# Kernel tuning notes

Hardware: AMD Instinct MI355X
Metric: run time of the kernel (lower is better)

## Reference

```python
import jax, jax.numpy as jnp
import numpy as np

N = 50000
E = 1600000
NEG_SLOPE = 0.2
BN_EPS = 1e-5


def gat_conv(x, src, dst, W, a_s, a_d, b):
    """PyG-style GATConv (concat=True). a_s/a_d: [H, C]."""
    H, C = a_s.shape
    h = (x @ W).reshape(-1, H, C)  # [N, H, C]
    alpha_src = jnp.einsum('nhc,hc->nh', h, a_s)  # [N, H]
    alpha_dst = jnp.einsum('nhc,hc->nh', h, a_d)  # [N, H]
    e = jax.nn.leaky_relu(alpha_src[src] + alpha_dst[dst], NEG_SLOPE)  # [E, H]
    # segment softmax over edges sharing the same destination node
    m = jax.ops.segment_max(e, dst, num_segments=N)
    e = jnp.exp(e - m[dst])
    s = jax.ops.segment_sum(e, dst, num_segments=N)
    alpha = e / (s[dst] + 1e-16)  # [E, H]
    msg = h[src] * alpha[:, :, None]  # [E, H, C]
    out = jax.ops.segment_sum(msg, dst, num_segments=N)  # [N, H, C]
    return out.reshape(-1, H * C) + b


def batch_norm(x, g, beta):
    mu = jnp.mean(x, axis=0)
    var = jnp.var(x, axis=0)
    return (x - mu) * jax.lax.rsqrt(var + BN_EPS) * g + beta


def setup_inputs() -> dict:
    key = jax.random.key(0)
    ks = jax.random.split(key, 20)
    d_in, hid, heads, d_out = 128, 16, 4, 40
    hh = hid * heads  # 64
    inp = {
        'x': jax.random.normal(ks[0], (N, d_in), jnp.float32),
        'edge_index': jax.random.randint(ks[1], (2, E), 0, N, jnp.int32),
        # layer 0: in -> hid*heads
        'W0': jax.random.normal(ks[2], (d_in, hh), jnp.float32) * 0.05,
        'a_src0': jax.random.normal(ks[3], (heads, hid), jnp.float32) * 0.05,
        'a_dst0': jax.random.normal(ks[4], (heads, hid), jnp.float32) * 0.05,
        'b0': jnp.zeros((hh,), jnp.float32),
        'g0': jnp.ones((hh,), jnp.float32),
        'beta0': jnp.zeros((hh,), jnp.float32),
        # layer 1: hid*heads -> hid*heads
        'W1': jax.random.normal(ks[5], (hh, hh), jnp.float32) * 0.1,
        'a_src1': jax.random.normal(ks[6], (heads, hid), jnp.float32) * 0.1,
        'a_dst1': jax.random.normal(ks[7], (heads, hid), jnp.float32) * 0.1,
        'b1': jnp.zeros((hh,), jnp.float32),
        'g1': jnp.ones((hh,), jnp.float32),
        'beta1': jnp.zeros((hh,), jnp.float32),
        # layer 2: hid*heads -> out, heads=1
        'W2': jax.random.normal(ks[8], (hh, d_out), jnp.float32) * 0.1,
        'a_src2': jax.random.normal(ks[9], (1, d_out), jnp.float32) * 0.1,
        'a_dst2': jax.random.normal(ks[10], (1, d_out), jnp.float32) * 0.1,
        'b2': jnp.zeros((d_out,), jnp.float32),
    }
    return inp


def reference(x, edge_index, W0, a_src0, a_dst0, b0, g0, beta0,
              W1, a_src1, a_dst1, b1, g1, beta1,
              W2, a_src2, a_dst2, b2):
    # add self-loops (PyG GATConv default)
    loop = jnp.arange(N, dtype=edge_index.dtype)
    src = jnp.concatenate([edge_index[0], loop])
    dst = jnp.concatenate([edge_index[1], loop])

    h = gat_conv(x, src, dst, W0, a_src0, a_dst0, b0)
    h = jax.nn.relu(batch_norm(h, g0, beta0))
    h = gat_conv(h, src, dst, W1, a_src1, a_dst1, b1)
    h = jax.nn.relu(batch_norm(h, g1, beta1))
    h = gat_conv(h, src, dst, W2, a_src2, a_dst2, b2)
    return jax.nn.log_softmax(h, axis=-1)
```

## Files before the change

kernel.cpp:

```cpp
#include <hip/hip_runtime.h>
#include <math.h>

#define NEG_SLOPE 0.2f
#define CAP 128
#define BCAP 6144

__device__ __forceinline__ unsigned enc_f(float f) {
    unsigned b = __float_as_uint(f);
    return (b & 0x80000000u) ? ~b : (b | 0x80000000u);
}
__device__ __forceinline__ float dec_f(unsigned u) {
    return (u & 0x80000000u) ? __uint_as_float(u ^ 0x80000000u) : __uint_as_float(~u);
}
#define ENC_NEG_INF 0x007FFFFFu

__device__ __forceinline__ unsigned short f2bf(float f) {
    unsigned u = __float_as_uint(f);
    u += 0x7fffu + ((u >> 16) & 1u);
    return (unsigned short)(u >> 16);
}
__device__ __forceinline__ float bf2f(unsigned short b) {
    return __uint_as_float(((unsigned)b) << 16);
}

static inline int nblk(long total, int b) { return (int)((total + b - 1) / b); }

__global__ void init_kernel(int* bincnt, float* bn, unsigned* menc, int nbin) {
    int i = blockIdx.x * blockDim.x + threadIdx.x;
    if (i < nbin) bincnt[i] = 0;
    if (i < 256) bn[i] = 0.f;
    if (i < 16) menc[i] = ENC_NEG_INF;
}

__global__ void bin_kernel(const int* __restrict__ srcs, const int* __restrict__ dsts,
                           int E_, int EA, int nbin, int* bincnt, unsigned* __restrict__ binbuf) {
    __shared__ int lh[512];
    __shared__ int lbase[512];
    int tid = threadIdx.x;
    for (int i = tid; i < nbin; i += 256) lh[i] = 0;
    __syncthreads();
    int chunk = (EA + gridDim.x - 1) / gridDim.x;
    int e0 = blockIdx.x * chunk;
    int e1 = e0 + chunk; if (e1 > EA) e1 = EA;
    for (int i = e0 + tid; i < e1; i += 256) {
        int d = (i < E_) ? dsts[i] : (i - E_);
        atomicAdd(&lh[d >> 7], 1);
    }
    __syncthreads();
    for (int i = tid; i < nbin; i += 256) {
        lbase[i] = atomicAdd(&bincnt[i], lh[i]);
        lh[i] = 0;
    }
    __syncthreads();
    for (int i = e0 + tid; i < e1; i += 256) {
        int s, d;
        if (i < E_) { s = srcs[i]; d = dsts[i]; } else { s = d = i - E_; }
        int b = d >> 7;
        int pos = lbase[b] + atomicAdd(&lh[b], 1);
        if (pos < BCAP) binbuf[(size_t)b * BCAP + pos] = ((unsigned)s << 16) | (unsigned)d;
    }
}

__global__ void build_kernel(const unsigned* __restrict__ binbuf, const int* __restrict__ bincnt,
                             unsigned short* __restrict__ esrc, int* __restrict__ cnt, int n) {
    __shared__ unsigned short slab[128 * CAP];
    __shared__ int lcnt[128];
    int tid = threadIdx.x;
    int b = blockIdx.x, d0 = b << 7;
    if (tid < 128) lcnt[tid] = 0;
    __syncthreads();
    int nb = bincnt[b]; if (nb > BCAP) nb = BCAP;
    for (int i = tid; i < nb; i += 256) {
        unsigned u = binbuf[(size_t)b * BCAP + i];
        int s = (int)(u >> 16);
        int ld = (int)(u & 0xffffu) - d0;
        int pos = atomicAdd(&lcnt[ld], 1);
        if (pos < CAP) slab[ld * CAP + pos] = (unsigned short)s;
    }
    __syncthreads();
    const uint4* sl = (const uint4*)slab;
    uint4* outp = (uint4*)esrc;
    for (int i = tid; i < 128 * CAP / 8; i += 256) {
        int r = i >> 4;
        if (d0 + r < n) outp[(size_t)(d0 + r) * (CAP / 8) + (i & 15)] = sl[i];
    }
    if (tid < 128 && d0 + tid < n) cnt[d0 + tid] = lcnt[tid];
}

template <int K, bool BN>
__global__ __launch_bounds__(256) void gemm_alpha_kernel(
    const float* __restrict__ X, const float* __restrict__ W,
    const float* __restrict__ a_s, const float* __restrict__ a_d,
    unsigned short* __restrict__ Hout, float* __restrict__ as_o,
    float* __restrict__ ad_o, unsigned* menc_, int n,
    const float* __restrict__ bnsum, const float* __restrict__ bnsq,
    const float* __restrict__ g, const float* __restrict__ beta) {
    __shared__ float Xs[32][132];
    __shared__ float Ws[32][64];
    __shared__ float scale[BN ? K : 4];
    __shared__ float shift[BN ? K : 4];
    __shared__ float redm[4][4];

    int tid = threadIdx.x;
    if (BN) {
        if (tid < K) {
            float inv_n = 1.0f / (float)n;
            float mu = bnsum[tid] * inv_n;
            float var = bnsq[tid] * inv_n - mu * mu;
            float sc = rsqrtf(var + 1e-5f) * g[tid];
            scale[tid] = sc;
            shift[tid] = beta[tid] - mu * sc;
        }
        __syncthreads();
    }

    int node0 = blockIdx.x * 128;
    int tx = tid & 7;
    int ty = tid >> 3;

    int snode = tid & 127;
    int khalf = (tid >> 7) * 16;
    int src_row = node0 + snode; if (src_row >= n) src_row = n - 1;
    const float* xrow = X + (size_t)src_row * K;

    float acc[4][8];
#pragma unroll
    for (int i = 0; i < 4; ++i)
#pragma unroll
        for (int j = 0; j < 8; ++j) acc[i][j] = 0.f;

    constexpr int NCH = K / 32;
    for (int c = 0; c < NCH; ++c) {
        int k0 = c * 32;
#pragma unroll
        for (int r = 0; r < 2; ++r) {
            int f = tid + r * 256;
            int kk = f >> 4;
            int cq = f & 15;
            float4 wv4 = *(const float4*)(W + (size_t)(k0 + kk) * 64 + cq * 4);
            *(float4*)&Ws[kk][cq * 4] = wv4;
        }
#pragma unroll
        for (int q = 0; q < 4; ++q) {
            int kk = khalf + q * 4;
            float4 v = *(const float4*)(xrow + k0 + kk);
            if (BN) {
                float4 sc = *(const float4*)(&scale[k0 + kk]);
                float4 sh = *(const float4*)(&shift[k0 + kk]);
                v.x = fmaxf(fmaf(v.x, sc.x, sh.x), 0.f);
                v.y = fmaxf(fmaf(v.y, sc.y, sh.y), 0.f);
                v.z = fmaxf(fmaf(v.z, sc.z, sh.z), 0.f);
                v.w = fmaxf(fmaf(v.w, sc.w, sh.w), 0.f);
            }
            Xs[kk + 0][snode] = v.x;
            Xs[kk + 1][snode] = v.y;
            Xs[kk + 2][snode] = v.z;
            Xs[kk + 3][snode] = v.w;
        }
        __syncthreads();
#pragma unroll 2
        for (int kk = 0; kk < 32; ++kk) {
            float4 xv = *(const float4*)(&Xs[kk][ty * 4]);
            float4 wa = *(const float4*)(&Ws[kk][tx * 8]);
            float4 wb = *(const float4*)(&Ws[kk][tx * 8 + 4]);
            float xs_[4] = {xv.x, xv.y, xv.z, xv.w};
            float ws_[8] = {wa.x, wa.y, wa.z, wa.w, wb.x, wb.y, wb.z, wb.w};
#pragma unroll
            for (int i = 0; i < 4; ++i)
#pragma unroll
                for (int j = 0; j < 8; ++j)
                    acc[i][j] = fmaf(xs_[i], ws_[j], acc[i][j]);
        }
        __syncthreads();
    }

    float4 asa = *(const float4*)(a_s + tx * 8);
    float4 asb = *(const float4*)(a_s + tx * 8 + 4);
    float4 ada = *(const float4*)(a_d + tx * 8);
    float4 adb = *(const float4*)(a_d + tx * 8 + 4);
    int head = tx >> 1;
    float p1v[4], p2v[4];
#pragma unroll
    for (int i = 0; i < 4; ++i) {
        float p1 = acc[i][0] * asa.x + acc[i][1] * asa.y + acc[i][2] * asa.z + acc[i][3] * asa.w
                 + acc[i][4] * asb.x + acc[i][5] * asb.y + acc[i][6] * asb.z + acc[i][7] * asb.w;
        float p2 = acc[i][0] * ada.x + acc[i][1] * ada.y + acc[i][2] * ada.z + acc[i][3] * ada.w
                 + acc[i][4] * adb.x + acc[i][5] * adb.y + acc[i][6] * adb.z + acc[i][7] * adb.w;
        p1 += __shfl_xor(p1, 1, 64);
        p2 += __shfl_xor(p2, 1, 64);
        p1v[i] = p1; p2v[i] = p2;
    }
#pragma unroll
    for (int i = 0; i < 4; ++i) {
        int node = node0 + ty * 4 + i;
        if (node < n) {
            unsigned r0 = (unsigned)f2bf(acc[i][0]) | ((unsigned)f2bf(acc[i][1]) << 16);
            unsigned r1 = (unsigned)f2bf(acc[i][2]) | ((unsigned)f2bf(acc[i][3]) << 16);
            unsigned r2 = (unsigned)f2bf(acc[i][4]) | ((unsigned)f2bf(acc[i][5]) << 16);
            unsigned r3 = (unsigned)f2bf(acc[i][6]) | ((unsigned)f2bf(acc[i][7]) << 16);
            *(uint4*)(Hout + (size_t)node * 64 + tx * 8) = make_uint4(r0, r1, r2, r3);
            if ((tx & 1) == 0) {
                as_o[(size_t)node * 4 + head] = p1v[i];
                ad_o[(size_t)node * 4 + head] = p2v[i];
            }
        }
    }
    float am = -1e30f;
    if ((tx & 1) == 0)
        am = fmaxf(fmaxf(p1v[0], p1v[1]), fmaxf(p1v[2], p1v[3]));
    am = fmaxf(am, __shfl_xor(am, 8, 64));
    am = fmaxf(am, __shfl_xor(am, 16, 64));
    am = fmaxf(am, __shfl_xor(am, 32, 64));
    int lane = tid & 63;
    if (lane < 8 && (lane & 1) == 0) redm[tid >> 6][lane >> 1] = am;
    __syncthreads();
    if (tid < 4) {
        float m = fmaxf(fmaxf(redm[0][tid], redm[1][tid]), fmaxf(redm[2][tid], redm[3][tid]));
        atomicMax(&menc_[tid], enc_f(m));
    }
}

__global__ void gather64_kernel(const int* __restrict__ cnt,
                                const unsigned short* __restrict__ esrc,
                                const float* __restrict__ as_, const float* __restrict__ ad_,
                                const unsigned short* __restrict__ Hf,
                                const unsigned* __restrict__ menc,
                                const float* __restrict__ bias, float* __restrict__ feat, int n) {
    int tid = threadIdx.x;
    int wv = tid >> 6, lane = tid & 63;
    int slot = lane >> 4, ql = lane & 15;
    int r8 = lane >> 3, qc = lane & 7;
    int node = blockIdx.x * 4 + wv;
    if (node >= n) return;

    int deg = cnt[node]; if (deg > CAP) deg = CAP;
    const unsigned short* ep = esrc + (size_t)node * CAP;
    float4 adv4 = *(const float4*)(ad_ + (size_t)node * 4);
    float adh = (slot == 0) ? adv4.x : (slot == 1) ? adv4.y : (slot == 2) ? adv4.z : adv4.w;
    float mm = dec_f(menc[slot]) + adh;
    float mh = mm > 0.f ? mm : NEG_SLOPE * mm;

    float4 accA = make_float4(0.f, 0.f, 0.f, 0.f);
    float4 accB = make_float4(0.f, 0.f, 0.f, 0.f);
    float wp = 0.f;
    int nch = (deg + 15) >> 4;

    int lim0 = deg < 16 ? deg : 16;
    int s0 = (ql < lim0) ? (int)ep[ql] : 0;
    float aA = as_[(unsigned)(s0 * 4 + slot)];
    int sA = 0;
    if (nch > 1) {
        int l1 = deg - 16; if (l1 > 16) l1 = 16;
        sA = (ql < l1) ? (int)ep[16 + ql] : 0;
    }
    uint4 hA0, hA1, hB0, hB1;
    {
        int sj0 = __shfl(s0, r8, 64);
        hA0 = *(const uint4*)(Hf + (unsigned)(sj0 * 64 + qc * 8));
        int sj1 = __shfl(s0, 8 + r8, 64);
        hA1 = *(const uint4*)(Hf + (unsigned)(sj1 * 64 + qc * 8));
    }
    hB0 = hA0; hB1 = hA1;
    int sB = 0; float aB = 0.f;

#define G64_FMA8(H0, WJ)                                                  \
    accA.x = fmaf(bf2f((unsigned short)(H0.x)), WJ, accA.x);              \
    accA.y = fmaf(bf2f((unsigned short)(H0.x >> 16)), WJ, accA.y);        \
    accA.z = fmaf(bf2f((unsigned short)(H0.y)), WJ, accA.z);              \
    accA.w = fmaf(bf2f((unsigned short)(H0.y >> 16)), WJ, accA.w);        \
    accB.x = fmaf(bf2f((unsigned short)(H0.z)), WJ, accB.x);              \
    accB.y = fmaf(bf2f((unsigned short)(H0.z >> 16)), WJ, accB.y);        \
    accB.z = fmaf(bf2f((unsigned short)(H0.w)), WJ, accB.z);              \
    accB.w = fmaf(bf2f((unsigned short)(H0.w >> 16)), WJ, accB.w);

#define G64_CHUNK(c, hC0, hC1, hN0, hN1, sC, sN, aC, aN)                      \
    {                                                                         \
        int lim = deg - (c) * 16; if (lim > 16) lim = 16;                     \
        float ev = aC + adh;                                                  \
        ev = ev > 0.f ? ev : NEG_SLOPE * ev;                                  \
        float w = (ql < lim) ? __expf(ev - mh) : 0.f;                         \
        if ((c) + 1 < nch) aN = as_[(unsigned)(sC * 4 + slot)];               \
        if ((c) + 2 < nch) {                                                  \
            int l2 = deg - ((c) + 2) * 16; if (l2 > 16) l2 = 16;              \
            sN = (ql < l2) ? (int)ep[((c) + 2) * 16 + ql] : 0;                \
        }                                                                     \
        if ((c) + 1 < nch) {                                                  \
            int sj0 = __shfl(sC, r8, 64);                                     \
            hN0 = *(const uint4*)(Hf + (unsigned)(sj0 * 64 + qc * 8));        \
            int sj1 = __shfl(sC, 8 + r8, 64);                                 \
            hN1 = *(const uint4*)(Hf + (unsigned)(sj1 * 64 + qc * 8));        \
        }                                                                     \
        wp += w;                                                              \
        {                                                                     \
            float wj = __shfl(w, ((qc >> 1) << 4) + r8, 64);                  \
            G64_FMA8(hC0, wj)                                                 \
        }                                                                     \
        if (lim > 8) {                                                        \
            float wj = __shfl(w, ((qc >> 1) << 4) + 8 + r8, 64);              \
            G64_FMA8(hC1, wj)                                                 \
        }                                                                     \
    }

    for (int c = 0; c < nch; c += 2) {
        G64_CHUNK(c, hA0, hA1, hB0, hB1, sA, sB, aA, aB);
        if (c + 1 < nch) G64_CHUNK(c + 1, hB0, hB1, hA0, hA1, sB, sA, aB, aA);
    }
#undef G64_CHUNK
#undef G64_FMA8

#pragma unroll
    for (int o = 8; o < 64; o <<= 1) {
        accA.x += __shfl_xor(accA.x, o, 64);
        accA.y += __shfl_xor(accA.y, o, 64);
        accA.z += __shfl_xor(accA.z, o, 64);
        accA.w += __shfl_xor(accA.w, o, 64);
        accB.x += __shfl_xor(accB.x, o, 64);
        accB.y += __shfl_xor(accB.y, o, 64);
        accB.z += __shfl_xor(accB.z, o, 64);
        accB.w += __shfl_xor(accB.w, o, 64);
    }
#pragma unroll
    for (int o = 1; o < 16; o <<= 1) wp += __shfl_xor(wp, o, 64);
    float wsh = __shfl(wp, ((lane & 7) >> 1) << 4, 64);
    if (lane < 8) {
        float inv = 1.0f / (wsh + 1e-16f);
        float4 bv0 = *(const float4*)(bias + lane * 8);
        float4 bv1 = *(const float4*)(bias + lane * 8 + 4);
        float4 r0, r1;
        r0.x = fmaf(accA.x, inv, bv0.x);
        r0.y = fmaf(accA.y, inv, bv0.y);
        r0.z = fmaf(accA.z, inv, bv0.z);
        r0.w = fmaf(accA.w, inv, bv0.w);
        r1.x = fmaf(accB.x, inv, bv1.x);
        r1.y = fmaf(accB.y, inv, bv1.y);
        r1.z = fmaf(accB.z, inv, bv1.z);
        r1.w = fmaf(accB.w, inv, bv1.w);
        *(float4*)(feat + (size_t)node * 64 + lane * 8) = r0;
        *(float4*)(feat + (size_t)node * 64 + lane * 8 + 4) = r1;
    }
}

__global__ void prep2_kernel(const float* __restrict__ feat, const float* __restrict__ bnsum,
                             const float* __restrict__ bnsq, const float* __restrict__ g,
                             const float* __restrict__ beta, const float* __restrict__ W2,
                             const float* __restrict__ as2v, const float* __restrict__ ad2v,
                             unsigned short* __restrict__ z, float* __restrict__ as_o,
                             float* __restrict__ ad_o, unsigned* menc_, int n) {
    __shared__ float sc[64], sh[64], vs[64], vd[64];
    int tid = threadIdx.x;
    if (tid < 64) {
        float inv_n = 1.0f / (float)n;
        float mu = bnsum[tid] * inv_n;
        float var = bnsq[tid] * inv_n - mu * mu;
        float s = rsqrtf(var + 1e-5f) * g[tid];
        sc[tid] = s;
        sh[tid] = beta[tid] - mu * s;
    } else if (tid < 128) {
        int k = tid - 64;
        float s1 = 0.f, s2 = 0.f;
        for (int j = 0; j < 40; ++j) {
            float wv = W2[k * 40 + j];
            s1 = fmaf(wv, as2v[j], s1);
            s2 = fmaf(wv, ad2v[j], s2);
        }
        vs[k] = s1;
        vd[k] = s2;
    }
    __syncthreads();
    int lane = tid & 63, wv = tid >> 6;
    float scl = sc[lane], shl = sh[lane], vsl = vs[lane], vdl = vd[lane];
    float amax = -1e30f;
    int nwaves = gridDim.x * 4;
    for (int node = blockIdx.x * 4 + wv; node < n; node += nwaves) {
        float v = fmaf(feat[(size_t)node * 64 + lane], scl, shl);
        v = v > 0.f ? v : 0.f;
        z[(size_t)node * 64 + lane] = f2bf(v);
        float p1 = v * vsl, p2 = v * vdl;
#pragma unroll
        for (int o = 1; o < 64; o <<= 1) {
            p1 += __shfl_xor(p1, o, 64);
            p2 += __shfl_xor(p2, o, 64);
        }
        amax = fmaxf(amax, p1);
        if (lane == 0) { as_o[node] = p1; ad_o[node] = p2; }
    }
    if (lane == 0) atomicMax(menc_, enc_f(amax));
}

__global__ void gatherz_kernel(const int* __restrict__ cnt,
                               const unsigned short* __restrict__ esrc,
                               const float* __restrict__ as_, const float* __restrict__ ad_,
                               const unsigned short* __restrict__ Z,
                               const unsigned* __restrict__ menc,
                               float* __restrict__ agg, int n) {
    int tid = threadIdx.x;
    int wv = tid >> 6, lane = tid & 63;
    int r8 = lane >> 3, qc = lane & 7;
    int node = blockIdx.x * 4 + wv;
    if (node >= n) return;

    int deg = cnt[node]; if (deg > CAP) deg = CAP;
    const unsigned short* ep = esrc + (size_t)node * CAP;
    float adv = ad_[node];
    float mm = dec_f(menc[0]) + adv;
    float mh = mm > 0.f ? mm : NEG_SLOPE * mm;

    float4 accA = make_float4(0.f, 0.f, 0.f, 0.f);
    float4 accB = make_float4(0.f, 0.f, 0.f, 0.f);
    float wp = 0.f;
    for (int base = 0; base < deg; base += 64) {
        int lim = deg - base; if (lim > 64) lim = 64;
        int s = 0;
        if (lane < lim) s = (int)ep[base + lane];
        float asv = (lane < lim) ? as_[(unsigned)s] : 0.f;
        uint4 hv[8];
#pragma unroll
        for (int i = 0; i < 8; ++i) {
            if (i * 8 >= lim) break;
            int sj = __shfl(s, i * 8 + r8, 64);
            hv[i] = *(const uint4*)(Z + (unsigned)(sj * 64 + qc * 8));
        }
        float w = 0.f;
        if (lane < lim) {
            float ev = asv + adv;
            ev = ev > 0.f ? ev : NEG_SLOPE * ev;
            w = __expf(ev - mh);
        }
        wp += w;
#pragma unroll
        for (int i = 0; i < 8; ++i) {
            if (i * 8 >= lim) break;
            float wj = __shfl(w, i * 8 + r8, 64);
            uint4 h4 = hv[i];
            accA.x = fmaf(bf2f((unsigned short)(h4.x)), wj, accA.x);
            accA.y = fmaf(bf2f((unsigned short)(h4.x >> 16)), wj, accA.y);
            accA.z = fmaf(bf2f((unsigned short)(h4.y)), wj, accA.z);
            accA.w = fmaf(bf2f((unsigned short)(h4.y >> 16)), wj, accA.w);
            accB.x = fmaf(bf2f((unsigned short)(h4.z)), wj, accB.x);
            accB.y = fmaf(bf2f((unsigned short)(h4.z >> 16)), wj, accB.y);
            accB.z = fmaf(bf2f((unsigned short)(h4.w)), wj, accB.z);
            accB.w = fmaf(bf2f((unsigned short)(h4.w >> 16)), wj, accB.w);
        }
    }
#pragma unroll
    for (int o = 8; o < 64; o <<= 1) {
        accA.x += __shfl_xor(accA.x, o, 64);
        accA.y += __shfl_xor(accA.y, o, 64);
        accA.z += __shfl_xor(accA.z, o, 64);
        accA.w += __shfl_xor(accA.w, o, 64);
        accB.x += __shfl_xor(accB.x, o, 64);
        accB.y += __shfl_xor(accB.y, o, 64);
        accB.z += __shfl_xor(accB.z, o, 64);
        accB.w += __shfl_xor(accB.w, o, 64);
    }
#pragma unroll
    for (int o = 1; o < 64; o <<= 1) wp += __shfl_xor(wp, o, 64);
    if (lane < 8) {
        float inv = 1.0f / (wp + 1e-16f);
        float4 r0, r1;
        r0.x = accA.x * inv; r0.y = accA.y * inv; r0.z = accA.z * inv; r0.w = accA.w * inv;
        r1.x = accB.x * inv; r1.y = accB.y * inv; r1.z = accB.z * inv; r1.w = accB.w * inv;
        *(float4*)(agg + (size_t)node * 64 + lane * 8) = r0;
        *(float4*)(agg + (size_t)node * 64 + lane * 8 + 4) = r1;
    }
}

__global__ __launch_bounds__(256) void gemm_lsm_kernel(const float* __restrict__ X,
                                                       const float* __restrict__ W,
                                                       const float* __restrict__ bias,
                                                       float* __restrict__ out, int n) {
    __shared__ float Xs[32][132];
    __shared__ float Ws[32][40];
    __shared__ float bs[40];
    int tid = threadIdx.x;
    if (tid < 40) bs[tid] = bias[tid];

    int node0 = blockIdx.x * 128;
    int tx = tid & 7;
    int ty = tid >> 3;
    int snode = tid & 127;
    int khalf = (tid >> 7) * 16;
    int src_row = node0 + snode; if (src_row >= n) src_row = n - 1;
    const float* xrow = X + (size_t)src_row * 64;

    float acc[4][5];
#pragma unroll
    for (int i = 0; i < 4; ++i)
#pragma unroll
        for (int j = 0; j < 5; ++j) acc[i][j] = 0.f;

    for (int c = 0; c < 2; ++c) {
        int k0 = c * 32;
        for (int f = tid; f < 320; f += 256) {
            int kk = f / 10, q = f - kk * 10;
            *(float4*)&Ws[kk][q * 4] = *(const float4*)(W + (size_t)(k0 + kk) * 40 + q * 4);
        }
#pragma unroll
        for (int q = 0; q < 4; ++q) {
            int kk = khalf + q * 4;
            float4 v = *(const float4*)(xrow + k0 + kk);
            Xs[kk + 0][snode] = v.x;
            Xs[kk + 1][snode] = v.y;
            Xs[kk + 2][snode] = v.z;
            Xs[kk + 3][snode] = v.w;
        }
        __syncthreads();
#pragma unroll 2
        for (int kk = 0; kk < 32; ++kk) {
            float4 xv = *(const float4*)(&Xs[kk][ty * 4]);
            float w0 = Ws[kk][tx * 5 + 0];
            float w1 = Ws[kk][tx * 5 + 1];
            float w2 = Ws[kk][tx * 5 + 2];
            float w3 = Ws[kk][tx * 5 + 3];
            float w4 = Ws[kk][tx * 5 + 4];
            float xs_[4] = {xv.x, xv.y, xv.z, xv.w};
#pragma unroll
            for (int i = 0; i < 4; ++i) {
                acc[i][0] = fmaf(xs_[i], w0, acc[i][0]);
                acc[i][1] = fmaf(xs_[i], w1, acc[i][1]);
                acc[i][2] = fmaf(xs_[i], w2, acc[i][2]);
                acc[i][3] = fmaf(xs_[i], w3, acc[i][3]);
                acc[i][4] = fmaf(xs_[i], w4, acc[i][4]);
            }
        }
        __syncthreads();
    }

    float b0 = bs[tx * 5 + 0], b1 = bs[tx * 5 + 1], b2 = bs[tx * 5 + 2],
          b3 = bs[tx * 5 + 3], b4 = bs[tx * 5 + 4];
#pragma unroll
    for (int i = 0; i < 4; ++i) {
        float v0 = acc[i][0] + b0, v1 = acc[i][1] + b1, v2 = acc[i][2] + b2,
              v3 = acc[i][3] + b3, v4 = acc[i][4] + b4;
        float m = fmaxf(fmaxf(fmaxf(v0, v1), fmaxf(v2, v3)), v4);
        m = fmaxf(m, __shfl_xor(m, 1, 64));
        m = fmaxf(m, __shfl_xor(m, 2, 64));
        m = fmaxf(m, __shfl_xor(m, 4, 64));
        float ex = __expf(v0 - m) + __expf(v1 - m) + __expf(v2 - m)
                 + __expf(v3 - m) + __expf(v4 - m);
        ex += __shfl_xor(ex, 1, 64);
        ex += __shfl_xor(ex, 2, 64);
        ex += __shfl_xor(ex, 4, 64);
        float ls = m + logf(ex);
        int node = node0 + ty * 4 + i;
        if (node < n) {
            float* op = out + (size_t)node * 40 + tx * 5;
            op[0] = v0 - ls;
            op[1] = v1 - ls;
            op[2] = v2 - ls;
            op[3] = v3 - ls;
            op[4] = v4 - ls;
        }
    }
}

__global__ void bn_stats_kernel(const float* __restrict__ feat, float* bnsum, float* bnsq,
                                int n) {
    __shared__ float ls[256], lq[256];
    int f = threadIdx.x & 63, y = threadIdx.x >> 6;
    float ps = 0.f, pq = 0.f;
    for (int node = blockIdx.x * 4 + y; node < n; node += gridDim.x * 4) {
        float v = feat[(size_t)node * 64 + f];
        ps += v;
        pq += v * v;
    }
    ls[threadIdx.x] = ps;
    lq[threadIdx.x] = pq;
    __syncthreads();
    if (y == 0) {
        atomicAdd(&bnsum[f], ls[f] + ls[f + 64] + ls[f + 128] + ls[f + 192]);
        atomicAdd(&bnsq[f], lq[f] + lq[f + 64] + lq[f + 128] + lq[f + 192]);
    }
}

extern "C" void kernel_launch(void* const* d_in, const int* in_sizes, int n_in,
                              void* d_out, int out_size, void* d_ws, size_t ws_size,
                              hipStream_t stream) {
    const float* x   = (const float*)d_in[0];
    const int*   ei  = (const int*)d_in[1];
    const float* W0  = (const float*)d_in[2];
    const float* as0 = (const float*)d_in[3];
    const float* ad0 = (const float*)d_in[4];
    const float* b0  = (const float*)d_in[5];
    const float* g0  = (const float*)d_in[6];
    const float* be0 = (const float*)d_in[7];
    const float* W1  = (const float*)d_in[8];
    const float* as1 = (const float*)d_in[9];
    const float* ad1 = (const float*)d_in[10];
    const float* b1  = (const float*)d_in[11];
    const float* g1  = (const float*)d_in[12];
    const float* be1 = (const float*)d_in[13];
    const float* W2  = (const float*)d_in[14];
    const float* as2 = (const float*)d_in[15];
    const float* ad2 = (const float*)d_in[16];
    const float* b2  = (const float*)d_in[17];

    const int N  = in_sizes[0] / 128;
    const int E  = in_sizes[1] / 2;
    const int EA = E + N;
    const int NBIN = (N + 127) >> 7;
    const int* srcs = ei;
    const int* dsts = ei + E;

    float* ws    = (float*)d_ws;
    float* feat  = ws;
    float* agg   = feat + (size_t)N * 64;
    float* asrc  = agg + (size_t)N * 64;
    float* adst  = asrc + (size_t)N * 4;
    float* bn    = adst + (size_t)N * 4;
    unsigned* menc = (unsigned*)(bn + 256);
    int* bincnt  = (int*)(menc + 16);
    int* cnt     = bincnt + 512;
    unsigned short* hb   = (unsigned short*)(cnt + N);
    unsigned short* esrc = hb + (size_t)N * 64;
    unsigned* binbuf = (unsigned*)(esrc + (size_t)N * CAP);

    float* bn0sum = bn, *bn0sq = bn + 64, *bn1sum = bn + 128, *bn1sq = bn + 192;

    init_kernel<<<2, 256, 0, stream>>>(bincnt, bn, menc, NBIN);
    bin_kernel<<<512, 256, 0, stream>>>(srcs, dsts, E, EA, NBIN, bincnt, binbuf);
    build_kernel<<<NBIN, 256, 0, stream>>>(binbuf, bincnt, esrc, cnt, N);

    gemm_alpha_kernel<128, false><<<nblk(N, 128), 256, 0, stream>>>(
        x, W0, as0, ad0, hb, asrc, adst, menc, N, nullptr, nullptr, nullptr, nullptr);
    gather64_kernel<<<nblk(N, 4), 256, 0, stream>>>(cnt, esrc, asrc, adst, hb, menc, b0, feat, N);
    bn_stats_kernel<<<512, 256, 0, stream>>>(feat, bn0sum, bn0sq, N);

    gemm_alpha_kernel<64, true><<<nblk(N, 128), 256, 0, stream>>>(
        feat, W1, as1, ad1, hb, asrc, adst, menc + 4, N, bn0sum, bn0sq, g0, be0);
    gather64_kernel<<<nblk(N, 4), 256, 0, stream>>>(cnt, esrc, asrc, adst, hb, menc + 4, b1,
                                                    feat, N);
    bn_stats_kernel<<<512, 256, 0, stream>>>(feat, bn1sum, bn1sq, N);

    prep2_kernel<<<512, 256, 0, stream>>>(feat, bn1sum, bn1sq, g1, be1, W2, as2, ad2,
                                          hb, asrc, adst, menc + 8, N);
    gatherz_kernel<<<nblk(N, 4), 256, 0, stream>>>(cnt, esrc, asrc, adst, hb, menc + 8, agg, N);
    gemm_lsm_kernel<<<nblk(N, 128), 256, 0, stream>>>(agg, W2, b2, (float*)d_out, N);
}
```

Baseline: 363.4 us.

## Replace two-pass binned CSR build with direct global-atomic scatter

```diff
diff --git a/kernel.cpp b/kernel.cpp
--- a/kernel.cpp
+++ b/kernel.cpp
@@ -3,7 +3,6 @@
 
 #define NEG_SLOPE 0.2f
 #define CAP 128
-#define BCAP 6144
 
 __device__ __forceinline__ unsigned enc_f(float f) {
     unsigned b = __float_as_uint(f);
@@ -25,66 +24,23 @@
 
 static inline int nblk(long total, int b) { return (int)((total + b - 1) / b); }
 
-__global__ void init_kernel(int* bincnt, float* bn, unsigned* menc, int nbin) {
-    int i = blockIdx.x * blockDim.x + threadIdx.x;
-    if (i < nbin) bincnt[i] = 0;
+__global__ void init_kernel(int* cnt, float* bn, unsigned* menc, int n) {
+    int i = blockIdx.x * 256 + threadIdx.x;
+    if (i < n) cnt[i] = 0;
     if (i < 256) bn[i] = 0.f;
     if (i < 16) menc[i] = ENC_NEG_INF;
 }
 
-__global__ void bin_kernel(const int* __restrict__ srcs, const int* __restrict__ dsts,
-                           int E_, int EA, int nbin, int* bincnt, unsigned* __restrict__ binbuf) {
-    __shared__ int lh[512];
-    __shared__ int lbase[512];
-    int tid = threadIdx.x;
-    for (int i = tid; i < nbin; i += 256) lh[i] = 0;
-    __syncthreads();
-    int chunk = (EA + gridDim.x - 1) / gridDim.x;
-    int e0 = blockIdx.x * chunk;
-    int e1 = e0 + chunk; if (e1 > EA) e1 = EA;
-    for (int i = e0 + tid; i < e1; i += 256) {
-        int d = (i < E_) ? dsts[i] : (i - E_);
-        atomicAdd(&lh[d >> 7], 1);
-    }
-    __syncthreads();
-    for (int i = tid; i < nbin; i += 256) {
-        lbase[i] = atomicAdd(&bincnt[i], lh[i]);
-        lh[i] = 0;
-    }
-    __syncthreads();
-    for (int i = e0 + tid; i < e1; i += 256) {
+__global__ void build_direct_kernel(const int* __restrict__ srcs, const int* __restrict__ dsts,
+                                    int E_, int EA, unsigned short* __restrict__ esrc,
+                                    int* cnt) {
+    int stride = gridDim.x * 256;
+    for (int i = blockIdx.x * 256 + threadIdx.x; i < EA; i += stride) {
         int s, d;
         if (i < E_) { s = srcs[i]; d = dsts[i]; } else { s = d = i - E_; }
-        int b = d >> 7;
-        int pos = lbase[b] + atomicAdd(&lh[b], 1);
-        if (pos < BCAP) binbuf[(size_t)b * BCAP + pos] = ((unsigned)s << 16) | (unsigned)d;
-    }
-}
-
-__global__ void build_kernel(const unsigned* __restrict__ binbuf, const int* __restrict__ bincnt,
-                             unsigned short* __restrict__ esrc, int* __restrict__ cnt, int n) {
-    __shared__ unsigned short slab[128 * CAP];
-    __shared__ int lcnt[128];
-    int tid = threadIdx.x;
-    int b = blockIdx.x, d0 = b << 7;
-    if (tid < 128) lcnt[tid] = 0;
-    __syncthreads();
-    int nb = bincnt[b]; if (nb > BCAP) nb = BCAP;
-    for (int i = tid; i < nb; i += 256) {
-        unsigned u = binbuf[(size_t)b * BCAP + i];
-        int s = (int)(u >> 16);
-        int ld = (int)(u & 0xffffu) - d0;
-        int pos = atomicAdd(&lcnt[ld], 1);
-        if (pos < CAP) slab[ld * CAP + pos] = (unsigned short)s;
-    }
-    __syncthreads();
-    const uint4* sl = (const uint4*)slab;
-    uint4* outp = (uint4*)esrc;
-    for (int i = tid; i < 128 * CAP / 8; i += 256) {
-        int r = i >> 4;
-        if (d0 + r < n) outp[(size_t)(d0 + r) * (CAP / 8) + (i & 15)] = sl[i];
-    }
-    if (tid < 128 && d0 + tid < n) cnt[d0 + tid] = lcnt[tid];
+        int pos = atomicAdd(&cnt[d], 1);
+        if (pos < CAP) esrc[(size_t)d * CAP + pos] = (unsigned short)s;
+    }
 }
 
 template <int K, bool BN>
@@ -598,7 +554,6 @@
     const int N  = in_sizes[0] / 128;
     const int E  = in_sizes[1] / 2;
     const int EA = E + N;
-    const int NBIN = (N + 127) >> 7;
     const int* srcs = ei;
     const int* dsts = ei + E;
 
@@ -609,17 +564,14 @@
     float* adst  = asrc + (size_t)N * 4;
     float* bn    = adst + (size_t)N * 4;
     unsigned* menc = (unsigned*)(bn + 256);
-    int* bincnt  = (int*)(menc + 16);
-    int* cnt     = bincnt + 512;
+    int* cnt     = (int*)(menc + 16);
     unsigned short* hb   = (unsigned short*)(cnt + N);
     unsigned short* esrc = hb + (size_t)N * 64;
-    unsigned* binbuf = (unsigned*)(esrc + (size_t)N * CAP);
 
     float* bn0sum = bn, *bn0sq = bn + 64, *bn1sum = bn + 128, *bn1sq = bn + 192;
 
-    init_kernel<<<2, 256, 0, stream>>>(bincnt, bn, menc, NBIN);
-    bin_kernel<<<512, 256, 0, stream>>>(srcs, dsts, E, EA, NBIN, bincnt, binbuf);
-    build_kernel<<<NBIN, 256, 0, stream>>>(binbuf, bincnt, esrc, cnt, N);
+    init_kernel<<<nblk(N, 256), 256, 0, stream>>>(cnt, bn, menc, N);
+    build_direct_kernel<<<2048, 256, 0, stream>>>(srcs, dsts, E, EA, esrc, cnt);
 
     gemm_alpha_kernel<128, false><<<nblk(N, 128), 256, 0, stream>>>(
         x, W0, as0, ad0, hb, asrc, adst, menc, N, nullptr, nullptr, nullptr, nullptr);
```

New measurement: 450.6 us. 24.0% more time.
